# Performance work log

Hardware: AMD Instinct MI355X
Metric: run time of the kernel (lower is better)

## Reference

```python
import jax, jax.numpy as jnp
import numpy as np

EMBED_DIM = 1024
NUM_HEADS = 16
HEAD_DIM = EMBED_DIM // NUM_HEADS


def setup_inputs() -> dict:
    key = jax.random.key(0)
    ks = jax.random.split(key, 7)
    B, S, E = 2, 2048, EMBED_DIM
    # xavier_uniform bound for square [E, E] weight
    bound = float(np.sqrt(6.0 / (E + E)))
    mkw = lambda k: jax.random.uniform(k, (E, E), jnp.float32, -bound, bound)
    return {
        "query": jax.random.normal(ks[0], (B, S, E), jnp.float32),
        "key": jax.random.normal(ks[1], (B, S, E), jnp.float32),
        "value": jax.random.normal(ks[2], (B, S, E), jnp.float32),
        "Wq": mkw(ks[3]),
        "Wk": mkw(ks[4]),
        "Wv": mkw(ks[5]),
        "Wo": mkw(ks[6]),
    }


def reference(query, key, value, Wq, Wk, Wv, Wo):
    # Chunked sigmoid attention: since sigmoid has no cross-key normalization
    # and all projections are bias-free linear maps, summing per-KV-chunk
    # partial outputs is mathematically identical to the full computation:
    #   out = (sigmoid(scale * Q K^T) @ V) @ Wo^T
    B, L, E = query.shape
    H, D = NUM_HEADS, HEAD_DIM
    scale = D ** -0.5
    q = (query @ Wq.T).reshape(B, L, H, D) * scale   # [B,L,H,D]
    k = (key @ Wk.T).reshape(B, -1, H, D)            # [B,S,H,D]
    v = (value @ Wv.T).reshape(B, -1, H, D)          # [B,S,H,D]
    scores = jax.nn.sigmoid(jnp.einsum('blhd,bshd->bhls', q, k))  # [B,H,L,S]
    o = jnp.einsum('bhls,bshd->blhd', scores, v).reshape(B, L, E)
    return o @ Wo.T
```

## Files before the change

### kernel.cpp

```cpp
#include <hip/hip_runtime.h>

typedef float f32x4 __attribute__((ext_vector_type(4)));
typedef float f32x16 __attribute__((ext_vector_type(16)));
typedef __bf16 bf16x4 __attribute__((ext_vector_type(4)));
typedef __bf16 bf16x8 __attribute__((ext_vector_type(8)));

constexpr int E = 1024;
constexpr int S = 2048;
constexpr int Bsz = 2;
constexpr int H = 16;
constexpr int Dh = 64;
constexpr int M = Bsz * S;
constexpr int E2 = 2048;

#define GLOAD_LDS16(g, l)                                                                 \
  __builtin_amdgcn_global_load_lds((const __attribute__((address_space(1))) void*)(g),    \
                                   (__attribute__((address_space(3))) void*)(l), 16, 0, 0)

__device__ __forceinline__ unsigned pk2(float a, float b) {
  union { __bf16 h[2]; unsigned u; } r;
  r.h[0] = (__bf16)a; r.h[1] = (__bf16)b;
  return r.u;
}

__global__ __launch_bounds__(256) void convert_bf16(
    const float* __restrict__ q, const float* __restrict__ k,
    const float* __restrict__ v, const float* __restrict__ wq,
    const float* __restrict__ wk, const float* __restrict__ wv,
    const float* __restrict__ wo, __bf16* __restrict__ aq,
    __bf16* __restrict__ ak, __bf16* __restrict__ av,
    __bf16* __restrict__ wqkv, __bf16* __restrict__ wob) {
  const int id = blockIdx.y;
  const float* src;
  __bf16* dst;
  int n;
  float scale = 1.0f;
  switch (id) {
    case 0: src = q;  dst = aq;             n = M * E; break;
    case 1: src = k;  dst = ak;             n = M * E; break;
    case 2: src = v;  dst = av;             n = M * E; break;
    case 3: src = wq; dst = wqkv;           n = E * E; scale = -0.18033688f; break;
    case 4: src = wk; dst = wqkv + E * E;   n = E * E; break;
    case 5: src = wv; dst = wqkv + 2 * E * E; n = E * E; break;
    default: src = wo; dst = wob;           n = E * E; break;
  }
  const int stride = gridDim.x * 256 * 8;
  for (int i = (blockIdx.x * 256 + threadIdx.x) * 8; i < n; i += stride) {
    f32x4 a = *reinterpret_cast<const f32x4*>(&src[i]);
    f32x4 b = *reinterpret_cast<const f32x4*>(&src[i + 4]);
    bf16x8 o;
    o[0] = (__bf16)(a[0] * scale); o[1] = (__bf16)(a[1] * scale);
    o[2] = (__bf16)(a[2] * scale); o[3] = (__bf16)(a[3] * scale);
    o[4] = (__bf16)(b[0] * scale); o[5] = (__bf16)(b[1] * scale);
    o[6] = (__bf16)(b[2] * scale); o[7] = (__bf16)(b[3] * scale);
    *reinterpret_cast<bf16x8*>(&dst[i]) = o;
  }
}

__global__ __launch_bounds__(256) void gemm_qkv(
    const __bf16* __restrict__ A0, const __bf16* __restrict__ A1,
    const __bf16* __restrict__ A2, const __bf16* __restrict__ Bw,
    __bf16* __restrict__ C0, __bf16* __restrict__ C1, __bf16* __restrict__ C2) {
  constexpr int NT  = 16;
  constexpr int NTN = 24;
  constexpr int NWG = 32 * NTN;
  constexpr int CPX = NWG / 8;

  __shared__ char smem[32768];

  const int t    = threadIdx.x;
  const int lane = t & 63;
  const int wid  = t >> 6;
  const int wr   = (wid >> 1) * 64;
  const int wc   = (wid & 1) * 64;
  const int r16  = lane & 15;

  const int bid = blockIdx.x;
  const int fid = (bid & 7) * CPX + (bid >> 3);
  const int mt  = fid / NTN;
  const int nt  = fid % NTN;
  const int tm  = mt * 128;
  const int tn  = nt * 128;
  const int which = tn >> 10;

  const __bf16* Ab = which == 0 ? A0 : which == 1 ? A1 : A2;

  auto stage = [&](int kt) {
    const int k0 = kt * 64;
#pragma unroll
    for (int c = wid; c < 32; c += 4) {
      const bool isA = c < 16;
      const int cc   = isA ? c : c - 16;
      const int L    = cc * 1024 + lane * 16;
      const int row  = L >> 7;
      const int sw   = ((L >> 4) & 7) ^ (row & 7);
      const __bf16* src = isA ? &Ab[(size_t)(tm + row) * 1024 + k0 + sw * 8]
                              : &Bw[(size_t)(tn + row) * 1024 + k0 + sw * 8];
      GLOAD_LDS16(src, smem + c * 1024);
    }
  };

  f32x4 acc[4][4] = {};

  for (int kt = 0; kt < NT; ++kt) {
    __syncthreads();
    stage(kt);
    __syncthreads();

    const char* As = smem;
    const char* Bs = smem + 16384;

#pragma unroll
    for (int kc = 0; kc < 2; ++kc) {
      bf16x8 af[4], bfv[4];
#pragma unroll
      for (int mi = 0; mi < 4; ++mi) {
        int row = wr + mi * 16 + r16;
        int g   = (kc * 4 + (lane >> 4)) ^ (row & 7);
        af[mi] = *reinterpret_cast<const bf16x8*>(As + row * 128 + g * 16);
      }
#pragma unroll
      for (int ni = 0; ni < 4; ++ni) {
        int row = wc + ni * 16 + r16;
        int g   = (kc * 4 + (lane >> 4)) ^ (row & 7);
        bfv[ni] = *reinterpret_cast<const bf16x8*>(Bs + row * 128 + g * 16);
      }
      __builtin_amdgcn_s_setprio(1);
#pragma unroll
      for (int mi = 0; mi < 4; ++mi)
#pragma unroll
        for (int ni = 0; ni < 4; ++ni)
          acc[mi][ni] = __builtin_amdgcn_mfma_f32_16x16x32_bf16(af[mi], bfv[ni],
                                                                acc[mi][ni], 0, 0, 0);
      __builtin_amdgcn_s_setprio(0);
    }
  }

#pragma unroll
  for (int mi = 0; mi < 4; ++mi) {
#pragma unroll
    for (int ni = 0; ni < 4; ++ni) {
#pragma unroll
      for (int j = 0; j < 4; ++j) {
        float v = acc[mi][ni][j];
        int m = tm + wr + mi * 16 + ((lane >> 4) << 2) + j;
        int n = tn + wc + ni * 16 + r16;
        int nl = n & 1023;
        int b = m >> 11, s = m & 2047, h = nl >> 6, d = nl & 63;
        __bf16* Cout = which == 0 ? C0 : which == 1 ? C1 : C2;
        if (which < 2) {
          Cout[((size_t)(b * H + h) * S + s) * Dh + d] = (__bf16)v;
        } else {
          int ssw = (s & ~12) | ((s & 4) << 1) | ((s & 8) >> 1);
          Cout[((size_t)(b * H + h) * Dh + d) * S + ssw] = (__bf16)v;
        }
      }
    }
  }
}

template <int TM, int MODE, int KS>
__global__ __launch_bounds__(256) void gemm_bf16nt(
    const __bf16* __restrict__ A0, const __bf16* __restrict__ A1,
    const __bf16* __restrict__ A2, const __bf16* __restrict__ Bw,
    void* __restrict__ C0, void* __restrict__ C1, void* __restrict__ C2) {
  static_assert(TM == 64, "vmcnt literal assumes TM=64 (6 chunks/wave)");
  constexpr int MI  = TM / 32;
  constexpr int NT  = KS / 64;
  constexpr int ACH = TM / 8;
  constexpr int NCH = ACH + 16;
  constexpr int NTN = 8;
  constexpr int NWG = NTN * (M / TM);
  constexpr int CPX = NWG / 8;

  __shared__ char smem[2][NCH * 1024];

  const int t    = threadIdx.x;
  const int lane = t & 63;
  const int wid  = t >> 6;
  const int wr   = (wid >> 1) * (TM / 2);
  const int wc   = (wid & 1) * 64;
  const int r16  = lane & 15;

  const int bid = blockIdx.x;
  const int fid = (bid & 7) * CPX + (bid >> 3);
  const int mt  = fid / NTN;
  const int nt  = fid % NTN;
  const int tm  = mt * TM;
  const int tn  = nt * 128;

  const __bf16* Ab = A0;

  auto stage = [&](int kt, int buf) {
    const int k0  = kt * 64;
    const int k0b = k0 & 1023;
    char* dst = smem[buf];
#pragma unroll
    for (int c = wid; c < NCH; c += 4) {
      const bool isA = c < ACH;
      const int cc   = isA ? c : c - ACH;
      const int L    = cc * 1024 + lane * 16;
      const int row  = L >> 7;
      const int sw   = ((L >> 4) & 7) ^ (row & 7);
      const __bf16* src = isA ? &Ab[(size_t)(tm + row) * KS + k0 + sw * 8]
                              : &Bw[(size_t)(tn + row) * 1024 + k0b + sw * 8];
      GLOAD_LDS16(src, dst + c * 1024);
    }
  };

  stage(0, 0);
  stage(1, 1);

  f32x4 acc[MI][4] = {};

  for (int kt = 0; kt < NT; ++kt) {
    const int buf = kt & 1;
    if (kt + 1 < NT) {
      asm volatile("s_waitcnt vmcnt(6)" ::: "memory");
    } else {
      asm volatile("s_waitcnt vmcnt(0)" ::: "memory");
    }
    __builtin_amdgcn_s_barrier();
    __builtin_amdgcn_sched_barrier(0);

    const __bf16* As = (const __bf16*)smem[buf];
    const __bf16* Bs = (const __bf16*)(smem[buf] + ACH * 1024);

#pragma unroll
    for (int kc = 0; kc < 2; ++kc) {
      bf16x8 af[MI], bfv[4];
#pragma unroll
      for (int mi = 0; mi < MI; ++mi) {
        int row = wr + mi * 16 + r16;
        int g   = (kc * 4 + (lane >> 4)) ^ (row & 7);
        af[mi] = *reinterpret_cast<const bf16x8*>(&As[row * 64 + g * 8]);
      }
#pragma unroll
      for (int ni = 0; ni < 4; ++ni) {
        int row = wc + ni * 16 + r16;
        int g   = (kc * 4 + (lane >> 4)) ^ (row & 7);
        bfv[ni] = *reinterpret_cast<const bf16x8*>(&Bs[row * 64 + g * 8]);
      }
      __builtin_amdgcn_s_setprio(1);
#pragma unroll
      for (int mi = 0; mi < MI; ++mi)
#pragma unroll
        for (int ni = 0; ni < 4; ++ni)
          acc[mi][ni] = __builtin_amdgcn_mfma_f32_16x16x32_bf16(af[mi], bfv[ni],
                                                                acc[mi][ni], 0, 0, 0);
      __builtin_amdgcn_s_setprio(0);
    }

    __builtin_amdgcn_sched_barrier(0);
    __builtin_amdgcn_s_barrier();
    if (kt + 2 < NT) stage(kt + 2, buf);
  }

#pragma unroll
  for (int mi = 0; mi < MI; ++mi) {
#pragma unroll
    for (int ni = 0; ni < 4; ++ni) {
#pragma unroll
      for (int j = 0; j < 4; ++j) {
        float v = acc[mi][ni][j];
        int m = tm + wr + mi * 16 + ((lane >> 4) << 2) + j;
        int n = tn + wc + ni * 16 + r16;
        ((float*)C0)[(size_t)m * E + n] = v;
      }
    }
  }
}

__global__ __launch_bounds__(64, 2) void attn_sigmoid(const __bf16* __restrict__ Q,
                                                      const __bf16* __restrict__ K,
                                                      const __bf16* __restrict__ Vt,
                                                      __bf16* __restrict__ O) {
  __shared__ char smem[16384];

  const int t    = threadIdx.x;
  const int lane = t & 63;
  const int l31  = lane & 31;
  const int hh   = lane >> 5;
  const int qt   = blockIdx.x >> 1;
  const int ss   = blockIdx.x & 1;
  const int q0   = qt * 64;
  const int h    = blockIdx.y;
  const int b    = blockIdx.z;

  const __bf16* Qh = Q + (size_t)(b * H + h) * S * Dh;
  const __bf16* Kh = K + (size_t)(b * H + h) * S * Dh;
  const __bf16* Vh = Vt + (size_t)(b * H + h) * Dh * S;

  const __bf16* kSrc = Kh + (size_t)(ss * 1024 + (lane >> 3)) * Dh +
                       (((lane & 7) ^ (lane >> 3)) * 8);
  const __bf16* vSrc = Vh + (size_t)(lane >> 2) * S + ss * 1024 +
                       (((lane & 3) ^ ((lane >> 3) & 3)) * 8);

  auto stage = [&](int it, int buf) {
    char* dst = smem + buf * 8192;
#pragma unroll
    for (int j = 0; j < 4; ++j)
      GLOAD_LDS16(kSrc + it * 2048 + j * 512, dst + j * 1024);
#pragma unroll
    for (int j = 0; j < 4; ++j)
      GLOAD_LDS16(vSrc + it * 32 + (size_t)j * 16 * S, dst + 4096 + j * 1024);
  };

  bf16x8 Qf[2][4];
#pragma unroll
  for (int g = 0; g < 2; ++g)
#pragma unroll
    for (int kc = 0; kc < 4; ++kc)
      Qf[g][kc] = *reinterpret_cast<const bf16x8*>(
          &Qh[(size_t)(q0 + g * 32 + l31) * Dh + kc * 16 + hh * 8]);

  stage(0, 0);
  stage(1, 1);

  const f32x16 ZERO = {};
  f32x16 ot[2][2] = {};

#pragma unroll 2
  for (int it = 0; it < 32; ++it) {
    const int buf = it & 1;
    if (it + 1 < 32) {
      asm volatile("s_waitcnt vmcnt(8)" ::: "memory");
    } else {
      asm volatile("s_waitcnt vmcnt(0)" ::: "memory");
    }
    __builtin_amdgcn_sched_barrier(0);

    const __bf16* Kb = (const __bf16*)(smem + buf * 8192);
    const __bf16* Vb = (const __bf16*)(smem + buf * 8192 + 4096);

    bf16x8 kf[4], vf[4];
#pragma unroll
    for (int kc = 0; kc < 4; ++kc) {
      int x = (2 * kc + hh) ^ (l31 & 7);
      kf[kc] = *reinterpret_cast<const bf16x8*>(&Kb[l31 * 64 + x * 8]);
    }
#pragma unroll
    for (int kc2 = 0; kc2 < 2; ++kc2)
#pragma unroll
      for (int dblk = 0; dblk < 2; ++dblk) {
        int row = dblk * 32 + l31;
        int x   = (2 * kc2 + hh) ^ ((l31 >> 1) & 3);
        vf[kc2 * 2 + dblk] = *reinterpret_cast<const bf16x8*>(&Vb[row * 32 + x * 8]);
      }
    asm volatile("s_waitcnt lgkmcnt(0)" ::: "memory");
    __builtin_amdgcn_sched_barrier(0);

    if (it + 2 < 32) stage(it + 2, buf);

    f32x16 s0, s1;
    __builtin_amdgcn_s_setprio(1);
    s0 = __builtin_amdgcn_mfma_f32_32x32x16_bf16(kf[0], Qf[0][0], ZERO, 0, 0, 0);
    s1 = __builtin_amdgcn_mfma_f32_32x32x16_bf16(kf[0], Qf[1][0], ZERO, 0, 0, 0);
#pragma unroll
    for (int kc = 1; kc < 4; ++kc) {
      s0 = __builtin_amdgcn_mfma_f32_32x32x16_bf16(kf[kc], Qf[0][kc], s0, 0, 0, 0);
      s1 = __builtin_amdgcn_mfma_f32_32x32x16_bf16(kf[kc], Qf[1][kc], s1, 0, 0, 0);
    }
    __builtin_amdgcn_s_setprio(0);

    bf16x8 F[2][2];
#pragma unroll
    for (int g = 0; g < 2; ++g) {
      union { unsigned u[4]; bf16x8 v; } fu[2];
#pragma unroll
      for (int kc2 = 0; kc2 < 2; ++kc2) {
#pragma unroll
        for (int jj = 0; jj < 4; ++jj) {
          float ya = g ? s1[kc2 * 8 + 2 * jj] : s0[kc2 * 8 + 2 * jj];
          float yb = g ? s1[kc2 * 8 + 2 * jj + 1] : s0[kc2 * 8 + 2 * jj + 1];
          float pa = __builtin_amdgcn_rcpf(1.0f + __builtin_amdgcn_exp2f(ya));
          float pb = __builtin_amdgcn_rcpf(1.0f + __builtin_amdgcn_exp2f(yb));
          fu[kc2].u[jj] = pk2(pa, pb);
        }
        F[g][kc2] = fu[kc2].v;
      }
    }

    __builtin_amdgcn_s_setprio(1);
#pragma unroll
    for (int kc2 = 0; kc2 < 2; ++kc2) {
#pragma unroll
      for (int dblk = 0; dblk < 2; ++dblk) {
        ot[0][dblk] = __builtin_amdgcn_mfma_f32_32x32x16_bf16(
            vf[kc2 * 2 + dblk], F[0][kc2], ot[0][dblk], 0, 0, 0);
        ot[1][dblk] = __builtin_amdgcn_mfma_f32_32x32x16_bf16(
            vf[kc2 * 2 + dblk], F[1][kc2], ot[1][dblk], 0, 0, 0);
      }
    }
    __builtin_amdgcn_s_setprio(0);
  }

  __syncthreads();
  __bf16* Os = (__bf16*)smem;
#pragma unroll
  for (int g = 0; g < 2; ++g) {
    int row = g * 32 + l31;
#pragma unroll
    for (int dblk = 0; dblk < 2; ++dblk)
#pragma unroll
      for (int rp = 0; rp < 4; ++rp) {
        int r  = rp * 4;
        int gg = dblk * 4 + rp;
        int by = row * 128 + ((gg ^ (row & 7)) * 16) + hh * 8;
        float a0 = ot[g][dblk][r];
        float a1 = ot[g][dblk][r + 1];
        float a2 = ot[g][dblk][r + 2];
        float a3 = ot[g][dblk][r + 3];
        unsigned long long val =
            (unsigned long long)pk2(a0, a1) | ((unsigned long long)pk2(a2, a3) << 32);
        *reinterpret_cast<unsigned long long*>((char*)Os + by) = val;
      }
  }
  __syncthreads();
#pragma unroll
  for (int i = 0; i < 8; ++i) {
    int c   = i * 64 + t;
    int row = c >> 3;
    int ch  = c & 7;
    bf16x8 v = *reinterpret_cast<const bf16x8*>(
        (char*)Os + row * 128 + ((ch ^ (row & 7)) * 16));
    *reinterpret_cast<bf16x8*>(
        &O[((size_t)(b * S) + q0 + row) * E2 + ss * 1024 + h * Dh + ch * 8]) = v;
  }
}

extern "C" void kernel_launch(void* const* d_in, const int* in_sizes, int n_in,
                              void* d_out, int out_size, void* d_ws, size_t ws_size,
                              hipStream_t stream) {
  const float* query = (const float*)d_in[0];
  const float* key_  = (const float*)d_in[1];
  const float* value = (const float*)d_in[2];
  const float* Wq    = (const float*)d_in[3];
  const float* Wk    = (const float*)d_in[4];
  const float* Wv    = (const float*)d_in[5];
  const float* Wo    = (const float*)d_in[6];

  char* ws = (char*)d_ws;
  __bf16* aq   = (__bf16*)(ws);
  __bf16* ak   = (__bf16*)(ws + ((size_t)8 << 20));
  __bf16* av   = (__bf16*)(ws + ((size_t)16 << 20));
  __bf16* wqkv = (__bf16*)(ws + ((size_t)24 << 20));
  __bf16* wob  = (__bf16*)(ws + ((size_t)30 << 20));
  __bf16* pq   = (__bf16*)(ws + ((size_t)32 << 20));
  __bf16* pk   = (__bf16*)(ws + ((size_t)40 << 20));
  __bf16* pvt  = (__bf16*)(ws + ((size_t)48 << 20));
  __bf16* ob   = (__bf16*)(ws);

  convert_bf16<<<dim3(512, 7), 256, 0, stream>>>(query, key_, value, Wq, Wk, Wv,
                                                 Wo, aq, ak, av, wqkv, wob);

  gemm_qkv<<<768, 256, 0, stream>>>(aq, ak, av, wqkv, pq, pk, pvt);

  attn_sigmoid<<<dim3(S / 32, H, Bsz), 64, 0, stream>>>(pq, pk, pvt, ob);

  gemm_bf16nt<64, 2, 2048><<<512, 256, 0, stream>>>(
      ob, nullptr, nullptr, wob, (float*)d_out, nullptr, nullptr);
}
```

Before: 132.7 us.

## Restructure attention to two-wave blocks over full KV, drop split-KV reduction in output GEMM

The attention kernel now uses 128-thread blocks in which each wave owns 32 query rows and walks the full 2048-key range, instead of splitting keys into two halves handled by separate blocks. The two waves share staged K/V tiles, with wave 0 loading K and wave 1 loading V, synchronised by barriers. Because there are no longer two partial outputs, the output projection GEMM runs with K=1024 instead of a concatenated 2048, halving its A reads and MACs. In exchange, each block iterates twice as long, the grid has half as many blocks, per-wave MFMA work per LDS load drops, and every iteration now carries barriers.

```diff
diff --git a/kernel.cpp b/kernel.cpp
--- a/kernel.cpp
+++ b/kernel.cpp
@@ -11,7 +11,6 @@
 constexpr int H = 16;
 constexpr int Dh = 64;
 constexpr int M = Bsz * S;
-constexpr int E2 = 2048;
 
 #define GLOAD_LDS16(g, l)                                                                 \
   __builtin_amdgcn_global_load_lds((const __attribute__((address_space(1))) void*)(g),    \
@@ -159,11 +158,10 @@
   }
 }
 
-template <int TM, int MODE, int KS>
+template <int TM, int KS>
 __global__ __launch_bounds__(256) void gemm_bf16nt(
-    const __bf16* __restrict__ A0, const __bf16* __restrict__ A1,
-    const __bf16* __restrict__ A2, const __bf16* __restrict__ Bw,
-    void* __restrict__ C0, void* __restrict__ C1, void* __restrict__ C2) {
+    const __bf16* __restrict__ A0, const __bf16* __restrict__ Bw,
+    float* __restrict__ C0) {
   static_assert(TM == 64, "vmcnt literal assumes TM=64 (6 chunks/wave)");
   constexpr int MI  = TM / 32;
   constexpr int NT  = KS / 64;
@@ -189,8 +187,6 @@
   const int tm  = mt * TM;
   const int tn  = nt * 128;
 
-  const __bf16* Ab = A0;
-
   auto stage = [&](int kt, int buf) {
     const int k0  = kt * 64;
     const int k0b = k0 & 1023;
@@ -202,7 +198,7 @@
       const int L    = cc * 1024 + lane * 16;
       const int row  = L >> 7;
       const int sw   = ((L >> 4) & 7) ^ (row & 7);
-      const __bf16* src = isA ? &Ab[(size_t)(tm + row) * KS + k0 + sw * 8]
+      const __bf16* src = isA ? &A0[(size_t)(tm + row) * KS + k0 + sw * 8]
                               : &Bw[(size_t)(tn + row) * 1024 + k0b + sw * 8];
       GLOAD_LDS16(src, dst + c * 1024);
     }
@@ -265,25 +261,24 @@
         float v = acc[mi][ni][j];
         int m = tm + wr + mi * 16 + ((lane >> 4) << 2) + j;
         int n = tn + wc + ni * 16 + r16;
-        ((float*)C0)[(size_t)m * E + n] = v;
-      }
-    }
-  }
-}
-
-__global__ __launch_bounds__(64, 2) void attn_sigmoid(const __bf16* __restrict__ Q,
-                                                      const __bf16* __restrict__ K,
-                                                      const __bf16* __restrict__ Vt,
-                                                      __bf16* __restrict__ O) {
+        C0[(size_t)m * E + n] = v;
+      }
+    }
+  }
+}
+
+__global__ __launch_bounds__(128, 4) void attn_sigmoid(const __bf16* __restrict__ Q,
+                                                       const __bf16* __restrict__ K,
+                                                       const __bf16* __restrict__ Vt,
+                                                       __bf16* __restrict__ O) {
   __shared__ char smem[16384];
 
   const int t    = threadIdx.x;
   const int lane = t & 63;
+  const int qgrp = t >> 6;
   const int l31  = lane & 31;
   const int hh   = lane >> 5;
-  const int qt   = blockIdx.x >> 1;
-  const int ss   = blockIdx.x & 1;
-  const int q0   = qt * 64;
+  const int q0   = blockIdx.x * 64;
   const int h    = blockIdx.y;
   const int b    = blockIdx.z;
 
@@ -291,43 +286,45 @@
   const __bf16* Kh = K + (size_t)(b * H + h) * S * Dh;
   const __bf16* Vh = Vt + (size_t)(b * H + h) * Dh * S;
 
-  const __bf16* kSrc = Kh + (size_t)(ss * 1024 + (lane >> 3)) * Dh +
+  const __bf16* kSrc = Kh + (size_t)(lane >> 3) * Dh +
                        (((lane & 7) ^ (lane >> 3)) * 8);
-  const __bf16* vSrc = Vh + (size_t)(lane >> 2) * S + ss * 1024 +
+  const __bf16* vSrc = Vh + (size_t)(lane >> 2) * S +
                        (((lane & 3) ^ ((lane >> 3) & 3)) * 8);
 
   auto stage = [&](int it, int buf) {
     char* dst = smem + buf * 8192;
-#pragma unroll
-    for (int j = 0; j < 4; ++j)
-      GLOAD_LDS16(kSrc + it * 2048 + j * 512, dst + j * 1024);
-#pragma unroll
-    for (int j = 0; j < 4; ++j)
-      GLOAD_LDS16(vSrc + it * 32 + (size_t)j * 16 * S, dst + 4096 + j * 1024);
+    if (qgrp == 0) {
+#pragma unroll
+      for (int j = 0; j < 4; ++j)
+        GLOAD_LDS16(kSrc + it * 2048 + j * 512, dst + j * 1024);
+    } else {
+#pragma unroll
+      for (int j = 0; j < 4; ++j)
+        GLOAD_LDS16(vSrc + it * 32 + (size_t)j * 16 * S, dst + 4096 + j * 1024);
+    }
   };
 
-  bf16x8 Qf[2][4];
-#pragma unroll
-  for (int g = 0; g < 2; ++g)
-#pragma unroll
-    for (int kc = 0; kc < 4; ++kc)
-      Qf[g][kc] = *reinterpret_cast<const bf16x8*>(
-          &Qh[(size_t)(q0 + g * 32 + l31) * Dh + kc * 16 + hh * 8]);
+  bf16x8 Qf[4];
+#pragma unroll
+  for (int kc = 0; kc < 4; ++kc)
+    Qf[kc] = *reinterpret_cast<const bf16x8*>(
+        &Qh[(size_t)(q0 + qgrp * 32 + l31) * Dh + kc * 16 + hh * 8]);
 
   stage(0, 0);
   stage(1, 1);
 
   const f32x16 ZERO = {};
-  f32x16 ot[2][2] = {};
+  f32x16 ot0 = {}, ot1 = {};
 
 #pragma unroll 2
-  for (int it = 0; it < 32; ++it) {
+  for (int it = 0; it < 64; ++it) {
     const int buf = it & 1;
-    if (it + 1 < 32) {
-      asm volatile("s_waitcnt vmcnt(8)" ::: "memory");
+    if (it + 1 < 64) {
+      asm volatile("s_waitcnt vmcnt(4)" ::: "memory");
     } else {
       asm volatile("s_waitcnt vmcnt(0)" ::: "memory");
     }
+    __builtin_amdgcn_s_barrier();
     __builtin_amdgcn_sched_barrier(0);
 
     const __bf16* Kb = (const __bf16*)(smem + buf * 8192);
@@ -347,70 +344,59 @@
         int x   = (2 * kc2 + hh) ^ ((l31 >> 1) & 3);
         vf[kc2 * 2 + dblk] = *reinterpret_cast<const bf16x8*>(&Vb[row * 32 + x * 8]);
       }
-    asm volatile("s_waitcnt lgkmcnt(0)" ::: "memory");
-    __builtin_amdgcn_sched_barrier(0);
-
-    if (it + 2 < 32) stage(it + 2, buf);
-
-    f32x16 s0, s1;
+
+    f32x16 sacc;
     __builtin_amdgcn_s_setprio(1);
-    s0 = __builtin_amdgcn_mfma_f32_32x32x16_bf16(kf[0], Qf[0][0], ZERO, 0, 0, 0);
-    s1 = __builtin_amdgcn_mfma_f32_32x32x16_bf16(kf[0], Qf[1][0], ZERO, 0, 0, 0);
-#pragma unroll
-    for (int kc = 1; kc < 4; ++kc) {
-      s0 = __builtin_amdgcn_mfma_f32_32x32x16_bf16(kf[kc], Qf[0][kc], s0, 0, 0, 0);
-      s1 = __builtin_amdgcn_mfma_f32_32x32x16_bf16(kf[kc], Qf[1][kc], s1, 0, 0, 0);
-    }
+    sacc = __builtin_amdgcn_mfma_f32_32x32x16_bf16(kf[0], Qf[0], ZERO, 0, 0, 0);
+#pragma unroll
+    for (int kc = 1; kc < 4; ++kc)
+      sacc = __builtin_amdgcn_mfma_f32_32x32x16_bf16(kf[kc], Qf[kc], sacc, 0, 0, 0);
     __builtin_amdgcn_s_setprio(0);
 
-    bf16x8 F[2][2];
-#pragma unroll
-    for (int g = 0; g < 2; ++g) {
+    bf16x8 F[2];
+    {
       union { unsigned u[4]; bf16x8 v; } fu[2];
 #pragma unroll
       for (int kc2 = 0; kc2 < 2; ++kc2) {
 #pragma unroll
         for (int jj = 0; jj < 4; ++jj) {
-          float ya = g ? s1[kc2 * 8 + 2 * jj] : s0[kc2 * 8 + 2 * jj];
-          float yb = g ? s1[kc2 * 8 + 2 * jj + 1] : s0[kc2 * 8 + 2 * jj + 1];
+          float ya = sacc[kc2 * 8 + 2 * jj];
+          float yb = sacc[kc2 * 8 + 2 * jj + 1];
           float pa = __builtin_amdgcn_rcpf(1.0f + __builtin_amdgcn_exp2f(ya));
           float pb = __builtin_amdgcn_rcpf(1.0f + __builtin_amdgcn_exp2f(yb));
           fu[kc2].u[jj] = pk2(pa, pb);
         }
-        F[g][kc2] = fu[kc2].v;
+        F[kc2] = fu[kc2].v;
       }
     }
 
     __builtin_amdgcn_s_setprio(1);
-#pragma unroll
-    for (int kc2 = 0; kc2 < 2; ++kc2) {
-#pragma unroll
-      for (int dblk = 0; dblk < 2; ++dblk) {
-        ot[0][dblk] = __builtin_amdgcn_mfma_f32_32x32x16_bf16(
-            vf[kc2 * 2 + dblk], F[0][kc2], ot[0][dblk], 0, 0, 0);
-        ot[1][dblk] = __builtin_amdgcn_mfma_f32_32x32x16_bf16(
-            vf[kc2 * 2 + dblk], F[1][kc2], ot[1][dblk], 0, 0, 0);
-      }
-    }
+    ot0 = __builtin_amdgcn_mfma_f32_32x32x16_bf16(vf[0], F[0], ot0, 0, 0, 0);
+    ot1 = __builtin_amdgcn_mfma_f32_32x32x16_bf16(vf[1], F[0], ot1, 0, 0, 0);
+    ot0 = __builtin_amdgcn_mfma_f32_32x32x16_bf16(vf[2], F[1], ot0, 0, 0, 0);
+    ot1 = __builtin_amdgcn_mfma_f32_32x32x16_bf16(vf[3], F[1], ot1, 0, 0, 0);
     __builtin_amdgcn_s_setprio(0);
+
+    __builtin_amdgcn_sched_barrier(0);
+    __builtin_amdgcn_s_barrier();
+    if (it + 2 < 64) stage(it + 2, buf);
   }
 
   __syncthreads();
   __bf16* Os = (__bf16*)smem;
-#pragma unroll
-  for (int g = 0; g < 2; ++g) {
-    int row = g * 32 + l31;
+  {
+    int row = qgrp * 32 + l31;
 #pragma unroll
     for (int dblk = 0; dblk < 2; ++dblk)
 #pragma unroll
       for (int rp = 0; rp < 4; ++rp) {
         int r  = rp * 4;
-        int gg = dblk * 4 + rp;
-        int by = row * 128 + ((gg ^ (row & 7)) * 16) + hh * 8;
-        float a0 = ot[g][dblk][r];
-        float a1 = ot[g][dblk][r + 1];
-        float a2 = ot[g][dblk][r + 2];
-        float a3 = ot[g][dblk][r + 3];
+        int g  = dblk * 4 + rp;
+        int by = row * 128 + ((g ^ (row & 7)) * 16) + hh * 8;
+        float a0 = dblk ? ot1[r]     : ot0[r];
+        float a1 = dblk ? ot1[r + 1] : ot0[r + 1];
+        float a2 = dblk ? ot1[r + 2] : ot0[r + 2];
+        float a3 = dblk ? ot1[r + 3] : ot0[r + 3];
         unsigned long long val =
             (unsigned long long)pk2(a0, a1) | ((unsigned long long)pk2(a2, a3) << 32);
         *reinterpret_cast<unsigned long long*>((char*)Os + by) = val;
@@ -418,14 +404,14 @@
   }
   __syncthreads();
 #pragma unroll
-  for (int i = 0; i < 8; ++i) {
-    int c   = i * 64 + t;
+  for (int i = 0; i < 4; ++i) {
+    int c   = i * 128 + t;
     int row = c >> 3;
     int ch  = c & 7;
     bf16x8 v = *reinterpret_cast<const bf16x8*>(
         (char*)Os + row * 128 + ((ch ^ (row & 7)) * 16));
     *reinterpret_cast<bf16x8*>(
-        &O[((size_t)(b * S) + q0 + row) * E2 + ss * 1024 + h * Dh + ch * 8]) = v;
+        &O[((size_t)(b * S) + q0 + row) * E + h * Dh + ch * 8]) = v;
   }
 }
 
@@ -456,8 +442,7 @@
 
   gemm_qkv<<<768, 256, 0, stream>>>(aq, ak, av, wqkv, pq, pk, pvt);
 
-  attn_sigmoid<<<dim3(S / 32, H, Bsz), 64, 0, stream>>>(pq, pk, pvt, ob);
-
-  gemm_bf16nt<64, 2, 2048><<<512, 256, 0, stream>>>(
-      ob, nullptr, nullptr, wob, (float*)d_out, nullptr, nullptr);
-}
+  attn_sigmoid<<<dim3(S / 64, H, Bsz), 128, 0, stream>>>(pq, pk, pvt, ob);
+
+  gemm_bf16nt<64, 1024><<<512, 256, 0, stream>>>(ob, wob, (float*)d_out);
+}
```

Result: slower. 136.5 us (+2.8%).
